# Optimization experiments

Measured on AMD Instinct MI355X. Metric: run time of the kernel, lower is better.

The kernel has to match this reference:

```python
import jax, jax.numpy as jnp
import numpy as np
from jax import lax

N = 14
K = 512
NUM_CLASSES = 10
TAO = 0.5 / (N * N)
BETA = 2.0


def make_t_p(n=N, tao=TAO, beta=BETA):
    # t_p[i, j, a, b] = tao * max(1 - beta * (|a-i| + |b-j|) / n, -1)
    idx = jnp.arange(n, dtype=jnp.float32)
    d = (jnp.abs(idx[:, None, None, None] - idx[None, None, :, None])
         + jnp.abs(idx[None, :, None, None] - idx[None, None, None, :]))
    return (tao * jnp.maximum(1.0 - beta * d / n, -1.0)).astype(jnp.float32)


def masked_output(x, t_p):
    # Vectorized equivalent of computeMaskedOutput: global spatial argmax per
    # (batch, channel) selects a template, then masked = relu(x * template).
    B, H, W, C = x.shape
    flat_idx = jnp.argmax(x.reshape(B, H * W, C), axis=1)      # [B, C]
    pi, pj = flat_idx // W, flat_idx % W
    tpl = t_p[pi, pj]                                          # [B, C, H, W]
    tpl = jnp.transpose(tpl, (0, 2, 3, 1))                     # [B, H, W, C]
    masked = jax.nn.relu(x * tpl)
    return masked, x, tpl


def compute_loss(x, pos_templates, act_sums, cls_sums, gt):
    # Fused segment-sum form of the original nested python loops.
    classes = jnp.zeros(NUM_CLASSES, x.dtype).at[gt].add(1.0)  # bincount
    cls_new = cls_sums + classes
    means = jnp.mean(x, axis=(1, 2))                           # [B, C]
    onehot = jax.nn.one_hot(gt, NUM_CLASSES, dtype=x.dtype)    # [B, 10]
    act_new = act_sums + means.T @ onehot                      # [C, 10]
    # divide_no_nan
    fm = jnp.where(cls_new[None, :] == 0, 0.0,
                   act_new / jnp.where(cls_new[None, :] == 0, 1.0, cls_new[None, :]))
    fclass = jnp.argmax(fm, axis=1)                            # [C]
    match = fclass[None, :] == gt[:, None]                     # [B, C]
    pt = jax.nn.relu(pos_templates)
    # relu(t_n) == 0 since t_n is strictly negative
    loss = jnp.where(match[:, None, None, :], pt, 0.0)
    return loss, act_new, cls_new


def forward(inputs, gt, conv_w, conv_b, dense_w, dense_b,
            activation_sums_1, activation_sums_2, class_sums_1, class_sums_2):
    t_p = make_t_p()
    raw_map = inputs  # base_model treated as identity on its feature map
    x1, X1_relu, pos_t1 = masked_output(raw_map, t_p)
    x3 = jax.nn.relu(lax.conv_general_dilated(
        x1, conv_w, window_strides=(1, 1), padding='SAME',
        dimension_numbers=('NHWC', 'HWIO', 'NHWC')) + conv_b)
    x2, X2_relu, pos_t2 = masked_output(x3, t_p)
    pooled = lax.reduce_window(x2, -jnp.inf, lax.max,
                               (1, 2, 2, 1), (1, 2, 2, 1), 'VALID')
    flat = pooled.reshape(pooled.shape[0], -1)
    probs = jax.nn.softmax(flat @ dense_w + dense_b, axis=-1)
    loss1, as1, cs1 = compute_loss(x1, pos_t1, activation_sums_1, class_sums_1, gt)
    loss2, as2, cs2 = compute_loss(x2, pos_t2, activation_sums_2, class_sums_2, gt)
    return probs, x1, x2, loss1, loss2, raw_map, pos_t1


def setup_inputs() -> dict:
    key = jax.random.key(0)
    ks = jax.random.split(key, 4)
    B = 128
    inputs = jax.random.uniform(ks[0], (B, N, N, K), dtype=jnp.float32)
    gt = jax.random.randint(ks[1], (B,), 0, NUM_CLASSES)
    conv_w = jax.random.normal(ks[2], (3, 3, K, K), dtype=jnp.float32) * 0.02
    conv_b = jnp.zeros((K,), jnp.float32)
    D = (N // 2) * (N // 2) * K  # 25088
    dense_w = jax.random.normal(ks[3], (D, NUM_CLASSES), dtype=jnp.float32) * 0.02
    dense_b = jnp.zeros((NUM_CLASSES,), jnp.float32)
    return {
        'inputs': inputs, 'gt': gt,
        'conv_w': conv_w, 'conv_b': conv_b,
        'dense_w': dense_w, 'dense_b': dense_b,
        'activation_sums_1': jnp.zeros((K, NUM_CLASSES), jnp.float32),
        'activation_sums_2': jnp.zeros((K, NUM_CLASSES), jnp.float32),
        'class_sums_1': jnp.zeros((NUM_CLASSES,), jnp.float32),
        'class_sums_2': jnp.zeros((NUM_CLASSES,), jnp.float32),
    }


def reference(inputs, gt, conv_w, conv_b, dense_w, dense_b,
              activation_sums_1, activation_sums_2, class_sums_1, class_sums_2):
    return forward(inputs, gt, conv_w, conv_b, dense_w, dense_b,
                   activation_sums_1, activation_sums_2,
                   class_sums_1, class_sums_2)
```

## Files before the change

### kernel.cpp

```cpp
#include <hip/hip_runtime.h>
#include <hip/hip_bf16.h>
#include <stdint.h>

#define TAO_F (0.5f/196.0f)
#define A_SC 512.0f
#define B_SC 64.0f
#define EPI (1.0f/32768.0f)

typedef float f32x4 __attribute__((ext_vector_type(4)));
typedef int   i32x4 __attribute__((ext_vector_type(4)));
typedef int   i32x8 __attribute__((ext_vector_type(8)));
typedef __attribute__((address_space(1))) const unsigned int u32_g;
typedef __attribute__((address_space(3))) unsigned int u32_l;

__device__ __forceinline__ void async_ld16(const void* g, void* l) {
  __builtin_amdgcn_global_load_lds((u32_g*)g, (u32_l*)l, 16, 0, 0);
}

__device__ __forceinline__ unsigned int pk_fp8x4(float a, float b, float c, float d) {
  int r = __builtin_amdgcn_cvt_pk_fp8_f32(a, b, 0, false);
  r = __builtin_amdgcn_cvt_pk_fp8_f32(c, d, r, true);
  return (unsigned int)r;
}

__device__ __forceinline__ void fuse1_body(
    int bid, const float* __restrict__ in, const int* __restrict__ gt,
    float* __restrict__ o_raw, float* __restrict__ o_x1, float* __restrict__ o_t1,
    uint8_t* __restrict__ x1p8, float* __restrict__ act1,
    int* __restrict__ idx1, uint8_t* smem) {
  int b = bid >> 4, cg = bid & 15;
  int t = threadIdx.x;
  int c4 = t & 7, sp = t >> 3;
  int c0 = cg * 32 + c4 * 4;
  int cq = c0 >> 2;
  float (*rv)[8][4] = (float(*)[8][4])smem;
  int   (*ri)[8][4] = (int(*)[8][4])(smem + 4096);

  const float4* ip = (const float4*)in + (size_t)b * 196 * 128;
  float4* rp = (float4*)o_raw + (size_t)b * 196 * 128;

  float bv[4] = {-1e30f, -1e30f, -1e30f, -1e30f};
  int bix[4] = {0, 0, 0, 0};
  for (int s = sp; s < 196; s += 32) {
    float4 v = ip[s * 128 + cq];
    rp[s * 128 + cq] = v;
    float vv[4] = {v.x, v.y, v.z, v.w};
#pragma unroll
    for (int k = 0; k < 4; ++k)
      if (vv[k] > bv[k]) { bv[k] = vv[k]; bix[k] = s; }
  }
#pragma unroll
  for (int k = 0; k < 4; ++k) { rv[sp][c4][k] = bv[k]; ri[sp][c4][k] = bix[k]; }
  __syncthreads();
  for (int st = 16; st >= 1; st >>= 1) {
    if (sp < st) {
#pragma unroll
      for (int k = 0; k < 4; ++k) {
        float v1 = rv[sp][c4][k], v2 = rv[sp + st][c4][k];
        int i1 = ri[sp][c4][k], i2 = ri[sp + st][c4][k];
        if (v2 > v1 || (v2 == v1 && i2 < i1)) { rv[sp][c4][k] = v2; ri[sp][c4][k] = i2; }
      }
    }
    __syncthreads();
  }
  int pi[4], pj[4];
#pragma unroll
  for (int k = 0; k < 4; ++k) {
    int id = ri[0][c4][k];
    pi[k] = id / 14; pj[k] = id - pi[k] * 14;
  }
  if (sp == 0)
    *(int4*)&idx1[b * 512 + c0] = make_int4(ri[0][c4][0], ri[0][c4][1], ri[0][c4][2], ri[0][c4][3]);
  __syncthreads();

  float4* xo = (float4*)o_x1 + (size_t)b * 196 * 128;
  float4* to = (float4*)o_t1 + (size_t)b * 196 * 128;
  float sm[4] = {0.f, 0.f, 0.f, 0.f};
  for (int s = sp; s < 196; s += 32) {
    int i = s / 14, j = s - i * 14;
    float4 x = ip[s * 128 + cq];
    float xx[4] = {x.x, x.y, x.z, x.w};
    float tp[4], mm[4];
#pragma unroll
    for (int k = 0; k < 4; ++k) {
      int di = i - pi[k]; di = di < 0 ? -di : di;
      int dj = j - pj[k]; dj = dj < 0 ? -dj : dj;
      tp[k] = TAO_F * fmaxf(1.0f - (float)(di + dj) * (1.0f / 7.0f), -1.0f);
      mm[k] = fmaxf(xx[k] * tp[k], 0.0f);
      sm[k] += mm[k];
    }
    xo[s * 128 + cq] = make_float4(mm[0], mm[1], mm[2], mm[3]);
    to[s * 128 + cq] = make_float4(tp[0], tp[1], tp[2], tp[3]);
    *(unsigned int*)&x1p8[((size_t)(b * 16 + i + 1) * 16 + (j + 1)) * 512 + c0] =
        pk_fp8x4(mm[0] * A_SC, mm[1] * A_SC, mm[2] * A_SC, mm[3] * A_SC);
  }
#pragma unroll
  for (int k = 0; k < 4; ++k) rv[sp][c4][k] = sm[k];
  __syncthreads();
  for (int st = 16; st >= 1; st >>= 1) {
    if (sp < st) {
#pragma unroll
      for (int k = 0; k < 4; ++k) rv[sp][c4][k] += rv[sp + st][c4][k];
    }
    __syncthreads();
  }
  if (sp == 0) {
    int g = gt[b];
#pragma unroll
    for (int k = 0; k < 4; ++k)
      atomicAdd(&act1[(c0 + k) * 10 + g], rv[0][c4][k] * (1.0f / 196.0f));
  }
}

__global__ __launch_bounds__(256) void k_pre(
    const float* __restrict__ w, uint8_t* __restrict__ wT8,
    const float* __restrict__ in, const int* __restrict__ gt,
    float* __restrict__ o_raw, float* __restrict__ o_x1, float* __restrict__ o_t1,
    uint8_t* __restrict__ x1p8, float* __restrict__ act1, int* __restrict__ idx1) {
  __shared__ uint8_t smem[16640];
  if (blockIdx.x < 576) {
    float (*tile)[65] = (float(*)[65])smem;
    int bid = blockIdx.x;
    int r = bid / 64; int rem = bid - r * 64;
    int cib = (rem >> 3) * 64, cob = (rem & 7) * 64;
    int tid = threadIdx.x;
    int col = tid & 63, rw = tid >> 6;
#pragma unroll
    for (int p = 0; p < 16; ++p) {
      int row = p * 4 + rw;
      tile[row][col] = w[(size_t)(r * 512 + cib + row) * 512 + cob + col];
    }
    __syncthreads();
    int cw = tid & 15, rw2 = tid >> 4;
#pragma unroll
    for (int p = 0; p < 4; ++p) {
      int co = p * 16 + rw2;
      unsigned int pk = pk_fp8x4(tile[cw * 4 + 0][co] * B_SC, tile[cw * 4 + 1][co] * B_SC,
                                 tile[cw * 4 + 2][co] * B_SC, tile[cw * 4 + 3][co] * B_SC);
      *(unsigned int*)&wT8[(size_t)(r * 512 + cob + co) * 512 + cib + cw * 4] = pk;
    }
  } else {
    fuse1_body(blockIdx.x - 576, in, gt, o_raw, o_x1, o_t1, x1p8, act1, idx1, smem);
  }
}

__global__ __launch_bounds__(256, 3) void k_gemm(const uint8_t* __restrict__ x1p8,
                                                 const uint8_t* __restrict__ wT8,
                                                 const float* __restrict__ conv_b,
                                                 float* __restrict__ x3) {
  int bid = blockIdx.x;
  int nt4 = bid & 3; int mt196 = bid >> 2;
  int m0 = mt196 * 128, co0 = nt4 * 128;
  int tid = threadIdx.x;
  int lane = tid & 63;

  __shared__ uint8_t As[128 * 128];
  __shared__ uint8_t Bs[128 * 128];

  int srow = tid >> 3;
  int sslot = tid & 7;
  int sx = (sslot ^ (srow & 7)) * 16;

  int baseA[4];
#pragma unroll
  for (int p = 0; p < 4; ++p) {
    int m = m0 + p * 32 + srow;
    int b = m / 196; int s = m - b * 196; int i = s / 14; int j = s - i * 14;
    baseA[p] = ((b * 16 + i + 1) * 16 + (j + 1)) * 512;
  }
  int baseB[4];
#pragma unroll
  for (int p = 0; p < 4; ++p) baseB[p] = (co0 + p * 32 + srow) * 512;

  f32x4 acc[4][4] = {};

  int m_off = (tid >> 7) * 64;
  int n_off = ((tid >> 6) & 1) * 64;
  int q = lane >> 4;
  int l16 = lane & 15;

  for (int r = 0; r < 9; ++r) {
    int offr = ((r / 3) * 16 + (r % 3) - 17) * 512;
    int wbase = r * 512 * 512;
    for (int cb = 0; cb < 4; ++cb) {
      int ko = cb * 128;
      __syncthreads();
#pragma unroll
      for (int p = 0; p < 4; ++p) {
        async_ld16(x1p8 + (baseA[p] + offr + ko + sx),
                   &As[(p * 32 + srow) * 128 + sslot * 16]);
        async_ld16(wT8 + (wbase + baseB[p] + ko + sx),
                   &Bs[(p * 32 + srow) * 128 + sslot * 16]);
      }
      __syncthreads();
      i32x8 af[4], bf[4];
#pragma unroll
      for (int tt = 0; tt < 4; ++tt) {
        int rowa = m_off + tt * 16 + l16;
        int e = rowa & 7;
        i32x4 lo = *(const i32x4*)&As[rowa * 128 + ((2 * q) ^ e) * 16];
        i32x4 hi = *(const i32x4*)&As[rowa * 128 + ((2 * q + 1) ^ e) * 16];
        af[tt] = (i32x8){lo.x, lo.y, lo.z, lo.w, hi.x, hi.y, hi.z, hi.w};
        int rowb = n_off + tt * 16 + l16;
        int eb = rowb & 7;
        i32x4 blo = *(const i32x4*)&Bs[rowb * 128 + ((2 * q) ^ eb) * 16];
        i32x4 bhi = *(const i32x4*)&Bs[rowb * 128 + ((2 * q + 1) ^ eb) * 16];
        bf[tt] = (i32x8){blo.x, blo.y, blo.z, blo.w, bhi.x, bhi.y, bhi.z, bhi.w};
      }
#pragma unroll
      for (int mt = 0; mt < 4; ++mt)
#pragma unroll
        for (int nt = 0; nt < 4; ++nt)
          acc[mt][nt] = __builtin_amdgcn_mfma_scale_f32_16x16x128_f8f6f4(
              af[mt], bf[nt], acc[mt][nt], 0, 0,
              0, 0x7F7F7F7F, 0, 0x7F7F7F7F);
    }
  }
#pragma unroll
  for (int nt = 0; nt < 4; ++nt) {
    int col = co0 + n_off + nt * 16 + l16;
    float bias = conv_b[col];
#pragma unroll
    for (int mt = 0; mt < 4; ++mt) {
      int mrow = m0 + m_off + mt * 16 + q * 4;
#pragma unroll
      for (int rg = 0; rg < 4; ++rg) {
        float v = acc[mt][nt][rg] * EPI + bias;
        x3[(size_t)(mrow + rg) * 512 + col] = fmaxf(v, 0.0f);
      }
    }
  }
}

__global__ __launch_bounds__(256) void k_fuse2(
    const float* __restrict__ x3, const int* __restrict__ gt,
    const float* __restrict__ dw, float* __restrict__ o_x2,
    float* __restrict__ act2, float* __restrict__ logits, int* __restrict__ idx2) {
  __shared__ float4 vals[196][8];
  __shared__ float rv[32][8][4];
  __shared__ int   ri[32][8][4];
  __shared__ float red[10];
  int bid = blockIdx.x; int b = bid >> 4, cg = bid & 15;
  int t = threadIdx.x, c4 = t & 7, sp = t >> 3;
  int c0 = cg * 32 + c4 * 4, cq = c0 >> 2;
  const float4* ip = (const float4*)x3 + (size_t)b * 196 * 128;

  float bv[4] = {-1e30f, -1e30f, -1e30f, -1e30f};
  int bix[4] = {0, 0, 0, 0};
  for (int s = sp; s < 196; s += 32) {
    float4 v = ip[s * 128 + cq];
    vals[s][c4] = v;
    float vv[4] = {v.x, v.y, v.z, v.w};
#pragma unroll
    for (int k = 0; k < 4; ++k)
      if (vv[k] > bv[k]) { bv[k] = vv[k]; bix[k] = s; }
  }
#pragma unroll
  for (int k = 0; k < 4; ++k) { rv[sp][c4][k] = bv[k]; ri[sp][c4][k] = bix[k]; }
  __syncthreads();
  for (int st = 16; st >= 1; st >>= 1) {
    if (sp < st) {
#pragma unroll
      for (int k = 0; k < 4; ++k) {
        float v1 = rv[sp][c4][k], v2 = rv[sp + st][c4][k];
        int i1 = ri[sp][c4][k], i2 = ri[sp + st][c4][k];
        if (v2 > v1 || (v2 == v1 && i2 < i1)) { rv[sp][c4][k] = v2; ri[sp][c4][k] = i2; }
      }
    }
    __syncthreads();
  }
  int pi[4], pj[4];
#pragma unroll
  for (int k = 0; k < 4; ++k) {
    int id = ri[0][c4][k];
    pi[k] = id / 14; pj[k] = id - pi[k] * 14;
  }
  if (sp == 0)
    *(int4*)&idx2[b * 512 + c0] = make_int4(ri[0][c4][0], ri[0][c4][1], ri[0][c4][2], ri[0][c4][3]);
  if (t < 10) red[t] = 0.f;
  __syncthreads();

  float4* xo = (float4*)o_x2 + (size_t)b * 196 * 128;
  float sm[4] = {0.f, 0.f, 0.f, 0.f};
  for (int s = sp; s < 196; s += 32) {
    int i = s / 14, j = s - i * 14;
    float4 x = vals[s][c4];
    float xx[4] = {x.x, x.y, x.z, x.w};
    float mm[4];
#pragma unroll
    for (int k = 0; k < 4; ++k) {
      int di = i - pi[k]; di = di < 0 ? -di : di;
      int dj = j - pj[k]; dj = dj < 0 ? -dj : dj;
      float tp = TAO_F * fmaxf(1.0f - (float)(di + dj) * (1.0f / 7.0f), -1.0f);
      mm[k] = fmaxf(xx[k] * tp, 0.0f);
      sm[k] += mm[k];
    }
    float4 m4 = make_float4(mm[0], mm[1], mm[2], mm[3]);
    xo[s * 128 + cq] = m4;
    vals[s][c4] = m4;
  }
#pragma unroll
  for (int k = 0; k < 4; ++k) rv[sp][c4][k] = sm[k];
  __syncthreads();
  for (int st = 16; st >= 1; st >>= 1) {
    if (sp < st) {
#pragma unroll
      for (int k = 0; k < 4; ++k) rv[sp][c4][k] += rv[sp + st][c4][k];
    }
    __syncthreads();
  }
  if (sp == 0) {
    int g = gt[b];
#pragma unroll
    for (int k = 0; k < 4; ++k)
      atomicAdd(&act2[(c0 + k) * 10 + g], rv[0][c4][k] * (1.0f / 196.0f));
  }

  float a[10] = {0.f,0.f,0.f,0.f,0.f,0.f,0.f,0.f,0.f,0.f};
  for (int pp = sp; pp < 49; pp += 32) {
    int ii = pp / 7, jj = pp - ii * 7;
    int s00 = (2 * ii) * 14 + 2 * jj;
    float4 v00 = vals[s00][c4], v01 = vals[s00 + 1][c4];
    float4 v10 = vals[s00 + 14][c4], v11 = vals[s00 + 15][c4];
    float pmx = fmaxf(fmaxf(v00.x, v01.x), fmaxf(v10.x, v11.x));
    float pmy = fmaxf(fmaxf(v00.y, v01.y), fmaxf(v10.y, v11.y));
    float pmz = fmaxf(fmaxf(v00.z, v01.z), fmaxf(v10.z, v11.z));
    float pmw = fmaxf(fmaxf(v00.w, v01.w), fmaxf(v10.w, v11.w));
    const float* wr = dw + ((size_t)((ii * 7 + jj) * 512 + c0)) * 10;
#pragma unroll
    for (int t2 = 0; t2 < 10; ++t2)
      a[t2] += pmx * wr[t2] + pmy * wr[10 + t2] + pmz * wr[20 + t2] + pmw * wr[30 + t2];
  }
  int lane = t & 63;
#pragma unroll
  for (int t2 = 0; t2 < 10; ++t2) {
    float v = a[t2];
    for (int off = 32; off > 0; off >>= 1) v += __shfl_down(v, off);
    if (lane == 0) atomicAdd(&red[t2], v);
  }
  __syncthreads();
  if (t < 10) atomicAdd(&logits[b * 10 + t], red[t]);
}

__global__ void k_stats(const float* __restrict__ act1, const float* __restrict__ act2,
                        const float* __restrict__ as1, const float* __restrict__ as2,
                        const float* __restrict__ cs1, const float* __restrict__ cs2,
                        const int* __restrict__ gt, const float* __restrict__ logits,
                        const float* __restrict__ db, int* __restrict__ fc1,
                        int* __restrict__ fc2, float* __restrict__ o_probs) {
  __shared__ int scnt[10];
  int tid = threadIdx.x;
  if (tid < 10) scnt[tid] = 0;
  __syncthreads();
  if (tid < 128) atomicAdd(&scnt[gt[tid]], 1);
  __syncthreads();
  int c = tid;
  float best1 = -1e30f, best2 = -1e30f; int b1 = 0, b2 = 0;
#pragma unroll
  for (int g = 0; g < 10; ++g) {
    float cnt = (float)scnt[g];
    float cn1 = cs1[g] + cnt;
    float cn2 = cs2[g] + cnt;
    float a1 = act1[c * 10 + g] + as1[c * 10 + g];
    float a2 = act2[c * 10 + g] + as2[c * 10 + g];
    float f1 = (cn1 == 0.f) ? 0.f : a1 / cn1;
    float f2 = (cn2 == 0.f) ? 0.f : a2 / cn2;
    if (f1 > best1) { best1 = f1; b1 = g; }
    if (f2 > best2) { best2 = f2; b2 = g; }
  }
  fc1[c] = b1; fc2[c] = b2;
  if (tid < 128) {
    float l[10]; float m = -1e30f;
#pragma unroll
    for (int t2 = 0; t2 < 10; ++t2) { l[t2] = logits[tid * 10 + t2] + db[t2]; m = fmaxf(m, l[t2]); }
    float s = 0.f;
#pragma unroll
    for (int t2 = 0; t2 < 10; ++t2) { l[t2] = expf(l[t2] - m); s += l[t2]; }
    float inv = 1.0f / s;
#pragma unroll
    for (int t2 = 0; t2 < 10; ++t2) o_probs[tid * 10 + t2] = l[t2] * inv;
  }
}

__global__ __launch_bounds__(256) void k_loss(
    const int* __restrict__ idx1, const int* __restrict__ idx2,
    const int* __restrict__ fc1, const int* __restrict__ fc2,
    const int* __restrict__ gt, float* __restrict__ o1, float* __restrict__ o2) {
  int bid = blockIdx.x;
  int b = bid / 14, i = bid - b * 14;
  int t = threadIdx.x;
  int cgp = t & 127, jh = t >> 7;
  int c0 = cgp * 4;
  int g = gt[b];
  int4 i1 = *(const int4*)&idx1[b * 512 + c0];
  int4 i2 = *(const int4*)&idx2[b * 512 + c0];
  int4 f1 = *(const int4*)&fc1[c0];
  int4 f2 = *(const int4*)&fc2[c0];
  float ms1[4] = {f1.x == g ? 1.f : 0.f, f1.y == g ? 1.f : 0.f,
                  f1.z == g ? 1.f : 0.f, f1.w == g ? 1.f : 0.f};
  float ms2[4] = {f2.x == g ? 1.f : 0.f, f2.y == g ? 1.f : 0.f,
                  f2.z == g ? 1.f : 0.f, f2.w == g ? 1.f : 0.f};
  int p1i[4], p1j[4], p2i[4], p2j[4];
  int ia1[4] = {i1.x, i1.y, i1.z, i1.w};
  int ia2[4] = {i2.x, i2.y, i2.z, i2.w};
#pragma unroll
  for (int k = 0; k < 4; ++k) {
    p1i[k] = ia1[k] / 14; p1j[k] = ia1[k] - p1i[k] * 14;
    p2i[k] = ia2[k] / 14; p2j[k] = ia2[k] - p2i[k] * 14;
  }
  float4* w1 = (float4*)o1 + ((size_t)b * 196 + i * 14) * 128 + (c0 >> 2);
  float4* w2 = (float4*)o2 + ((size_t)b * 196 + i * 14) * 128 + (c0 >> 2);
  for (int jj = 0; jj < 7; ++jj) {
    int j = jh * 7 + jj;
    float r1[4], r2[4];
#pragma unroll
    for (int k = 0; k < 4; ++k) {
      int d1i = i - p1i[k]; d1i = d1i < 0 ? -d1i : d1i;
      int d1j = j - p1j[k]; d1j = d1j < 0 ? -d1j : d1j;
      int d2i = i - p2i[k]; d2i = d2i < 0 ? -d2i : d2i;
      int d2j = j - p2j[k]; d2j = d2j < 0 ? -d2j : d2j;
      r1[k] = ms1[k] * (TAO_F * fmaxf(1.0f - (float)(d1i + d1j) * (1.0f / 7.0f), 0.0f));
      r2[k] = ms2[k] * (TAO_F * fmaxf(1.0f - (float)(d2i + d2j) * (1.0f / 7.0f), 0.0f));
    }
    w1[(size_t)j * 128] = make_float4(r1[0], r1[1], r1[2], r1[3]);
    w2[(size_t)j * 128] = make_float4(r2[0], r2[1], r2[2], r2[3]);
  }
}

extern "C" void kernel_launch(void* const* d_in, const int* in_sizes, int n_in,
                              void* d_out, int out_size, void* d_ws, size_t ws_size,
                              hipStream_t stream) {
  const float* inputs  = (const float*)d_in[0];
  const int*   gt      = (const int*)d_in[1];
  const float* conv_w  = (const float*)d_in[2];
  const float* conv_b  = (const float*)d_in[3];
  const float* dense_w = (const float*)d_in[4];
  const float* dense_b = (const float*)d_in[5];
  const float* as1     = (const float*)d_in[6];
  const float* as2     = (const float*)d_in[7];
  const float* cs1     = (const float*)d_in[8];
  const float* cs2     = (const float*)d_in[9];

  float* out = (float*)d_out;
  const size_t S = 12845056;
  float* o_probs = out;
  float* o_x1  = out + 1280;
  float* o_x2  = o_x1 + S;
  float* o_l1  = o_x2 + S;
  float* o_l2  = o_l1 + S;
  float* o_raw = o_l2 + S;
  float* o_t1  = o_raw + S;

  uint8_t* w8 = (uint8_t*)d_ws;
  uint8_t* x1p8 = w8;
  float*   x3   = (float*)(w8 + 16777216);
  uint8_t* wT8  = w8 + 68157440;
  int*   idx1 = (int*)(w8 + 70516736);
  int*   idx2 = (int*)(w8 + 70778880);
  float* act1 = (float*)(w8 + 71041024);
  float* act2 = (float*)(w8 + 71061504);
  float* logits = (float*)(w8 + 71081984);
  int*   fc1  = (int*)(w8 + 71087104);
  int*   fc2  = (int*)(w8 + 71089152);

  hipMemsetAsync(x1p8, 0, 16777216, stream);
  hipMemsetAsync(act1, 0, 46080, stream);

  k_pre   <<<576 + 2048, 256, 0, stream>>>(conv_w, wT8, inputs, gt, o_raw, o_x1, o_t1,
                                           x1p8, act1, idx1);
  k_gemm  <<<784, 256, 0, stream>>>(x1p8, wT8, conv_b, x3);
  k_fuse2 <<<2048, 256, 0, stream>>>(x3, gt, dense_w, o_x2, act2, logits, idx2);
  k_stats <<<1, 512, 0, stream>>>(act1, act2, as1, as2, cs1, cs2, gt, logits, dense_b,
                                  fc1, fc2, o_probs);
  k_loss  <<<1792, 256, 0, stream>>>(idx1, idx2, fc1, fc2, gt, o_l1, o_l2);
}
```

Baseline: 546.6 us.

## Fuse stats into loss kernel, zero only padding borders, cache inputs in LDS

Removes the full 16MB memset of the padded fp8 activation buffer and instead zeroes only the halo rows and columns in extra k_pre blocks, since the interior is overwritten. Merges the single-block k_stats kernel into the loss kernel, with every block recomputing the per-channel class argmax into shared memory, which removes one launch and a serialized one-block step. Also stores the input tile in LDS during the argmax pass so the masking pass reads it from shared memory instead of re-reading global memory. The costs are doubled LDS per block in k_pre, which may lower occupancy, and redundant stats computation in all 1792 loss blocks.

```diff
diff --git a/kernel.cpp b/kernel.cpp
--- a/kernel.cpp
+++ b/kernel.cpp
@@ -24,17 +24,18 @@
 }
 
 __device__ __forceinline__ void fuse1_body(
-    int bid, const float* __restrict__ in, const int* __restrict__ gt,
+    int lb, const float* __restrict__ in, const int* __restrict__ gt,
     float* __restrict__ o_raw, float* __restrict__ o_x1, float* __restrict__ o_t1,
     uint8_t* __restrict__ x1p8, float* __restrict__ act1,
     int* __restrict__ idx1, uint8_t* smem) {
-  int b = bid >> 4, cg = bid & 15;
+  int b = lb >> 4, cgi = lb & 15;
   int t = threadIdx.x;
   int c4 = t & 7, sp = t >> 3;
-  int c0 = cg * 32 + c4 * 4;
+  int c0 = cgi * 32 + c4 * 4;
   int cq = c0 >> 2;
-  float (*rv)[8][4] = (float(*)[8][4])smem;
-  int   (*ri)[8][4] = (int(*)[8][4])(smem + 4096);
+  float4 (*vals)[8] = (float4(*)[8])smem;
+  float (*rv)[8][4] = (float(*)[8][4])(smem + 25088);
+  int   (*ri)[8][4] = (int(*)[8][4])(smem + 29184);
 
   const float4* ip = (const float4*)in + (size_t)b * 196 * 128;
   float4* rp = (float4*)o_raw + (size_t)b * 196 * 128;
@@ -44,6 +45,7 @@
   for (int s = sp; s < 196; s += 32) {
     float4 v = ip[s * 128 + cq];
     rp[s * 128 + cq] = v;
+    vals[s][c4] = v;
     float vv[4] = {v.x, v.y, v.z, v.w};
 #pragma unroll
     for (int k = 0; k < 4; ++k)
@@ -70,7 +72,8 @@
     pi[k] = id / 14; pj[k] = id - pi[k] * 14;
   }
   if (sp == 0)
-    *(int4*)&idx1[b * 512 + c0] = make_int4(ri[0][c4][0], ri[0][c4][1], ri[0][c4][2], ri[0][c4][3]);
+    *(int4*)&idx1[b * 512 + c0] =
+        make_int4(ri[0][c4][0], ri[0][c4][1], ri[0][c4][2], ri[0][c4][3]);
   __syncthreads();
 
   float4* xo = (float4*)o_x1 + (size_t)b * 196 * 128;
@@ -78,7 +81,7 @@
   float sm[4] = {0.f, 0.f, 0.f, 0.f};
   for (int s = sp; s < 196; s += 32) {
     int i = s / 14, j = s - i * 14;
-    float4 x = ip[s * 128 + cq];
+    float4 x = vals[s][c4];
     float xx[4] = {x.x, x.y, x.z, x.w};
     float tp[4], mm[4];
 #pragma unroll
@@ -117,30 +120,45 @@
     const float* __restrict__ in, const int* __restrict__ gt,
     float* __restrict__ o_raw, float* __restrict__ o_x1, float* __restrict__ o_t1,
     uint8_t* __restrict__ x1p8, float* __restrict__ act1, int* __restrict__ idx1) {
-  __shared__ uint8_t smem[16640];
-  if (blockIdx.x < 576) {
+  __shared__ uint8_t smem[33280];
+  int bid = blockIdx.x, tid = threadIdx.x;
+  if (bid < 576) {
     float (*tile)[65] = (float(*)[65])smem;
-    int bid = blockIdx.x;
     int r = bid / 64; int rem = bid - r * 64;
     int cib = (rem >> 3) * 64, cob = (rem & 7) * 64;
-    int tid = threadIdx.x;
     int col = tid & 63, rw = tid >> 6;
 #pragma unroll
-    for (int p = 0; p < 16; ++p) {
-      int row = p * 4 + rw;
+    for (int u = 0; u < 16; ++u) {
+      int row = u * 4 + rw;
       tile[row][col] = w[(size_t)(r * 512 + cib + row) * 512 + cob + col];
     }
     __syncthreads();
     int cw = tid & 15, rw2 = tid >> 4;
 #pragma unroll
-    for (int p = 0; p < 4; ++p) {
-      int co = p * 16 + rw2;
+    for (int u = 0; u < 4; ++u) {
+      int co = u * 16 + rw2;
       unsigned int pk = pk_fp8x4(tile[cw * 4 + 0][co] * B_SC, tile[cw * 4 + 1][co] * B_SC,
                                  tile[cw * 4 + 2][co] * B_SC, tile[cw * 4 + 3][co] * B_SC);
       *(unsigned int*)&wT8[(size_t)(r * 512 + cob + co) * 512 + cib + cw * 4] = pk;
     }
+  } else if (bid < 704) {
+    int b = bid - 576;
+    uint8_t* img = x1p8 + (size_t)b * 16 * 16 * 512;
+    int4 z = make_int4(0, 0, 0, 0);
+    for (int idx = tid; idx < 1920; idx += 256) {
+      size_t off;
+      if (idx < 512) off = (size_t)idx * 16;
+      else if (idx < 1024) off = (size_t)15 * 16 * 512 + (idx - 512) * 16;
+      else {
+        int r2 = idx - 1024;
+        int seg = r2 >> 5, o = r2 & 31;
+        int i = (seg >> 1) + 1, j = (seg & 1) ? 15 : 0;
+        off = ((size_t)i * 16 + j) * 512 + o * 16;
+      }
+      *(int4*)(img + off) = z;
+    }
   } else {
-    fuse1_body(blockIdx.x - 576, in, gt, o_raw, o_x1, o_t1, x1p8, act1, idx1, smem);
+    fuse1_body(bid - 704, in, gt, o_raw, o_x1, o_t1, x1p8, act1, idx1, smem);
   }
 }
 
@@ -163,14 +181,14 @@
 
   int baseA[4];
 #pragma unroll
-  for (int p = 0; p < 4; ++p) {
-    int m = m0 + p * 32 + srow;
+  for (int u = 0; u < 4; ++u) {
+    int m = m0 + u * 32 + srow;
     int b = m / 196; int s = m - b * 196; int i = s / 14; int j = s - i * 14;
-    baseA[p] = ((b * 16 + i + 1) * 16 + (j + 1)) * 512;
+    baseA[u] = ((b * 16 + i + 1) * 16 + (j + 1)) * 512;
   }
   int baseB[4];
 #pragma unroll
-  for (int p = 0; p < 4; ++p) baseB[p] = (co0 + p * 32 + srow) * 512;
+  for (int u = 0; u < 4; ++u) baseB[u] = (co0 + u * 32 + srow) * 512;
 
   f32x4 acc[4][4] = {};
 
@@ -186,11 +204,11 @@
       int ko = cb * 128;
       __syncthreads();
 #pragma unroll
-      for (int p = 0; p < 4; ++p) {
-        async_ld16(x1p8 + (baseA[p] + offr + ko + sx),
-                   &As[(p * 32 + srow) * 128 + sslot * 16]);
-        async_ld16(wT8 + (wbase + baseB[p] + ko + sx),
-                   &Bs[(p * 32 + srow) * 128 + sslot * 16]);
+      for (int u = 0; u < 4; ++u) {
+        async_ld16(x1p8 + (baseA[u] + offr + ko + sx),
+                   &As[(u * 32 + srow) * 128 + sslot * 16]);
+        async_ld16(wT8 + (wbase + baseB[u] + ko + sx),
+                   &Bs[(u * 32 + srow) * 128 + sslot * 16]);
       }
       __syncthreads();
       i32x8 af[4], bf[4];
@@ -240,9 +258,9 @@
   __shared__ float rv[32][8][4];
   __shared__ int   ri[32][8][4];
   __shared__ float red[10];
-  int bid = blockIdx.x; int b = bid >> 4, cg = bid & 15;
+  int bid = blockIdx.x; int b = bid >> 4, cgi = bid & 15;
   int t = threadIdx.x, c4 = t & 7, sp = t >> 3;
-  int c0 = cg * 32 + c4 * 4, cq = c0 >> 2;
+  int c0 = cgi * 32 + c4 * 4, cq = c0 >> 2;
   const float4* ip = (const float4*)x3 + (size_t)b * 196 * 128;
 
   float bv[4] = {-1e30f, -1e30f, -1e30f, -1e30f};
@@ -276,7 +294,8 @@
     pi[k] = id / 14; pj[k] = id - pi[k] * 14;
   }
   if (sp == 0)
-    *(int4*)&idx2[b * 512 + c0] = make_int4(ri[0][c4][0], ri[0][c4][1], ri[0][c4][2], ri[0][c4][3]);
+    *(int4*)&idx2[b * 512 + c0] =
+        make_int4(ri[0][c4][0], ri[0][c4][1], ri[0][c4][2], ri[0][c4][3]);
   if (t < 10) red[t] = 0.f;
   __syncthreads();
 
@@ -342,34 +361,40 @@
   if (t < 10) atomicAdd(&logits[b * 10 + t], red[t]);
 }
 
-__global__ void k_stats(const float* __restrict__ act1, const float* __restrict__ act2,
-                        const float* __restrict__ as1, const float* __restrict__ as2,
-                        const float* __restrict__ cs1, const float* __restrict__ cs2,
-                        const int* __restrict__ gt, const float* __restrict__ logits,
-                        const float* __restrict__ db, int* __restrict__ fc1,
-                        int* __restrict__ fc2, float* __restrict__ o_probs) {
+__global__ __launch_bounds__(256) void k_post(
+    const int* __restrict__ idx1, const int* __restrict__ idx2,
+    const float* __restrict__ act1, const float* __restrict__ act2,
+    const float* __restrict__ as1, const float* __restrict__ as2,
+    const float* __restrict__ cs1, const float* __restrict__ cs2,
+    const int* __restrict__ gt, const float* __restrict__ logits,
+    const float* __restrict__ db, float* __restrict__ o_probs,
+    float* __restrict__ o_l1, float* __restrict__ o_l2) {
+  __shared__ int fcs1[512], fcs2[512];
   __shared__ int scnt[10];
+  int bid = blockIdx.x;
   int tid = threadIdx.x;
   if (tid < 10) scnt[tid] = 0;
   __syncthreads();
   if (tid < 128) atomicAdd(&scnt[gt[tid]], 1);
   __syncthreads();
-  int c = tid;
-  float best1 = -1e30f, best2 = -1e30f; int b1 = 0, b2 = 0;
-#pragma unroll
-  for (int g = 0; g < 10; ++g) {
-    float cnt = (float)scnt[g];
-    float cn1 = cs1[g] + cnt;
-    float cn2 = cs2[g] + cnt;
-    float a1 = act1[c * 10 + g] + as1[c * 10 + g];
-    float a2 = act2[c * 10 + g] + as2[c * 10 + g];
-    float f1 = (cn1 == 0.f) ? 0.f : a1 / cn1;
-    float f2 = (cn2 == 0.f) ? 0.f : a2 / cn2;
-    if (f1 > best1) { best1 = f1; b1 = g; }
-    if (f2 > best2) { best2 = f2; b2 = g; }
-  }
-  fc1[c] = b1; fc2[c] = b2;
-  if (tid < 128) {
+  for (int c = tid; c < 512; c += 256) {
+    float best1 = -1e30f, best2 = -1e30f; int b1 = 0, b2 = 0;
+#pragma unroll
+    for (int g = 0; g < 10; ++g) {
+      float cnt = (float)scnt[g];
+      float cn1 = cs1[g] + cnt;
+      float cn2 = cs2[g] + cnt;
+      float a1 = act1[c * 10 + g] + as1[c * 10 + g];
+      float a2 = act2[c * 10 + g] + as2[c * 10 + g];
+      float f1 = (cn1 == 0.f) ? 0.f : a1 / cn1;
+      float f2 = (cn2 == 0.f) ? 0.f : a2 / cn2;
+      if (f1 > best1) { best1 = f1; b1 = g; }
+      if (f2 > best2) { best2 = f2; b2 = g; }
+    }
+    fcs1[c] = b1; fcs2[c] = b2;
+  }
+  __syncthreads();
+  if (bid == 0 && tid < 128) {
     float l[10]; float m = -1e30f;
 #pragma unroll
     for (int t2 = 0; t2 < 10; ++t2) { l[t2] = logits[tid * 10 + t2] + db[t2]; m = fmaxf(m, l[t2]); }
@@ -380,26 +405,18 @@
 #pragma unroll
     for (int t2 = 0; t2 < 10; ++t2) o_probs[tid * 10 + t2] = l[t2] * inv;
   }
-}
-
-__global__ __launch_bounds__(256) void k_loss(
-    const int* __restrict__ idx1, const int* __restrict__ idx2,
-    const int* __restrict__ fc1, const int* __restrict__ fc2,
-    const int* __restrict__ gt, float* __restrict__ o1, float* __restrict__ o2) {
-  int bid = blockIdx.x;
   int b = bid / 14, i = bid - b * 14;
-  int t = threadIdx.x;
-  int cgp = t & 127, jh = t >> 7;
+  int cgp = tid & 127, jh = tid >> 7;
   int c0 = cgp * 4;
   int g = gt[b];
   int4 i1 = *(const int4*)&idx1[b * 512 + c0];
   int4 i2 = *(const int4*)&idx2[b * 512 + c0];
-  int4 f1 = *(const int4*)&fc1[c0];
-  int4 f2 = *(const int4*)&fc2[c0];
-  float ms1[4] = {f1.x == g ? 1.f : 0.f, f1.y == g ? 1.f : 0.f,
-                  f1.z == g ? 1.f : 0.f, f1.w == g ? 1.f : 0.f};
-  float ms2[4] = {f2.x == g ? 1.f : 0.f, f2.y == g ? 1.f : 0.f,
-                  f2.z == g ? 1.f : 0.f, f2.w == g ? 1.f : 0.f};
+  float ms1[4], ms2[4];
+#pragma unroll
+  for (int k = 0; k < 4; ++k) {
+    ms1[k] = (fcs1[c0 + k] == g) ? 1.f : 0.f;
+    ms2[k] = (fcs2[c0 + k] == g) ? 1.f : 0.f;
+  }
   int p1i[4], p1j[4], p2i[4], p2j[4];
   int ia1[4] = {i1.x, i1.y, i1.z, i1.w};
   int ia2[4] = {i2.x, i2.y, i2.z, i2.w};
@@ -408,8 +425,8 @@
     p1i[k] = ia1[k] / 14; p1j[k] = ia1[k] - p1i[k] * 14;
     p2i[k] = ia2[k] / 14; p2j[k] = ia2[k] - p2i[k] * 14;
   }
-  float4* w1 = (float4*)o1 + ((size_t)b * 196 + i * 14) * 128 + (c0 >> 2);
-  float4* w2 = (float4*)o2 + ((size_t)b * 196 + i * 14) * 128 + (c0 >> 2);
+  float4* w1 = (float4*)o_l1 + ((size_t)b * 196 + i * 14) * 128 + (c0 >> 2);
+  float4* w2 = (float4*)o_l2 + ((size_t)b * 196 + i * 14) * 128 + (c0 >> 2);
   for (int jj = 0; jj < 7; ++jj) {
     int j = jh * 7 + jj;
     float r1[4], r2[4];
@@ -460,17 +477,13 @@
   float* act1 = (float*)(w8 + 71041024);
   float* act2 = (float*)(w8 + 71061504);
   float* logits = (float*)(w8 + 71081984);
-  int*   fc1  = (int*)(w8 + 71087104);
-  int*   fc2  = (int*)(w8 + 71089152);
-
-  hipMemsetAsync(x1p8, 0, 16777216, stream);
+
   hipMemsetAsync(act1, 0, 46080, stream);
 
-  k_pre   <<<576 + 2048, 256, 0, stream>>>(conv_w, wT8, inputs, gt, o_raw, o_x1, o_t1,
-                                           x1p8, act1, idx1);
+  k_pre   <<<2752, 256, 0, stream>>>(conv_w, wT8, inputs, gt, o_raw, o_x1, o_t1,
+                                     x1p8, act1, idx1);
   k_gemm  <<<784, 256, 0, stream>>>(x1p8, wT8, conv_b, x3);
   k_fuse2 <<<2048, 256, 0, stream>>>(x3, gt, dense_w, o_x2, act2, logits, idx2);
-  k_stats <<<1, 512, 0, stream>>>(act1, act2, as1, as2, cs1, cs2, gt, logits, dense_b,
-                                  fc1, fc2, o_probs);
-  k_loss  <<<1792, 256, 0, stream>>>(idx1, idx2, fc1, fc2, gt, o_l1, o_l2);
-}
+  k_post  <<<1792, 256, 0, stream>>>(idx1, idx2, act1, act2, as1, as2, cs1, cs2,
+                                     gt, logits, dense_b, o_probs, o_l1, o_l2);
+}
```

Measured after the change: 565.7 us. 1.03x slower.
